# Kernel tuning notes

Measured on AMD Instinct MI355X. Metric: run time of the kernel, lower is better.

The kernel has to match this reference:

```python
import jax, jax.numpy as jnp
import numpy as np

IOU_THR = 0.5
SCORE_THR = 0.05
K = 1000  # fixed NMS candidate budget (padded-ragged replacement for data-dependent shapes)
BBOX_XFORM_CLIP = float(np.log(1000.0 / 16.0))  # torchvision BoxCoder clamp


def setup_inputs() -> dict:
    key = jax.random.key(0)
    k1, k2, k3, k4 = jax.random.split(key, 4)
    B, N, C = 8, 50000, 80
    pred_labels = jax.random.normal(k1, (B, N, C), jnp.float32)
    pred_bboxes = 0.5 * jax.random.normal(k2, (B, N, 4), jnp.float32)
    # anchors: valid xyxy boxes on a ~640px image
    cxy = jax.random.uniform(k3, (B, N, 2), jnp.float32, minval=0.0, maxval=640.0)
    wh = jax.random.uniform(k4, (B, N, 2), jnp.float32, minval=8.0, maxval=128.0)
    anchors = jnp.concatenate([cxy - 0.5 * wh, cxy + 0.5 * wh], axis=-1)
    return {"pred_labels": pred_labels, "pred_bboxes": pred_bboxes, "anchors": anchors}


def _decode_boxes(codes, anchors):
    # torchvision BoxCoder.decode_single with weights (1,1,1,1)
    w = anchors[:, 2] - anchors[:, 0]
    h = anchors[:, 3] - anchors[:, 1]
    cx = anchors[:, 0] + 0.5 * w
    cy = anchors[:, 1] + 0.5 * h
    dx, dy = codes[:, 0], codes[:, 1]
    dw = jnp.minimum(codes[:, 2], BBOX_XFORM_CLIP)
    dh = jnp.minimum(codes[:, 3], BBOX_XFORM_CLIP)
    pcx = dx * w + cx
    pcy = dy * h + cy
    pw = jnp.exp(dw) * w
    ph = jnp.exp(dh) * h
    return jnp.stack([pcx - 0.5 * pw, pcy - 0.5 * ph, pcx + 0.5 * pw, pcy + 0.5 * ph], axis=-1)


def _pairwise_iou(b):
    # b: [K,4] xyxy
    area = (b[:, 2] - b[:, 0]) * (b[:, 3] - b[:, 1])
    lt = jnp.maximum(b[:, None, :2], b[None, :, :2])
    rb = jnp.minimum(b[:, None, 2:], b[None, :, 2:])
    wh = jnp.clip(rb - lt, 0.0)
    inter = wh[..., 0] * wh[..., 1]
    return inter / (area[:, None] + area[None, :] - inter + 1e-9)


def _nms_keep(boxes):
    # boxes already sorted by descending score; greedy suppression
    iou = _pairwise_iou(boxes)
    idx = jnp.arange(K)

    def body(i, keep):
        suppress = (iou[i] > IOU_THR) & (idx > i) & keep[i]
        return keep & ~suppress

    return jax.lax.fori_loop(0, K, body, jnp.ones((K,), bool))


def _decode_image(labels, codes, anchors):
    # labels [N,C], codes [N,4], anchors [N,4]
    probs = jax.nn.sigmoid(labels)
    dt_score = jnp.max(probs, axis=1)
    dt_class = jnp.argmax(probs, axis=1)
    fg = (dt_class != 0) & (dt_score > SCORE_THR)
    masked = jnp.where(fg, dt_score, -1.0)  # background sorts last
    top_s, top_i = jax.lax.top_k(masked, K)
    cls = dt_class[top_i]
    boxes = _decode_boxes(codes[top_i], anchors[top_i])
    keep = _nms_keep(boxes) & (top_s > 0.0)
    out_scores = jnp.where(keep, top_s, 0.0)
    out_boxes = jnp.where(keep[:, None], boxes, 0.0)
    out_cls = jnp.where(keep, cls, -1)
    return out_cls, out_scores, out_boxes, keep


def reference(pred_labels, pred_bboxes, anchors):
    # Padded-ragged analog of the nested_tensor result:
    # category_ids [B,K] int, scores [B,K], bboxes [B,K,4], keep [B,K] validity mask
    return jax.vmap(_decode_image)(pred_labels, pred_bboxes, anchors)
```

## Files before the change

kernel.cpp:

```cpp
#include <hip/hip_runtime.h>
#include <cstdint>
#include <cstddef>

typedef unsigned int u32;
typedef unsigned long long u64;

#define BB   8
#define NN   50000
#define CC   80
#define KTOP 1000
#define CAP  4096
#define NHB  129
#define CLIPV 4.135166556742356f

#define OFF_KEYS 0UL
#define OFF_CLS  1600000UL
#define OFF_HIST 3200000UL
#define OFF_CNT  3204128UL
#define OFF_CAND 3204640UL
#define OFF_TKEY 3466784UL
#define OFF_TIDX 3498784UL
#define OFF_BOX  3530784UL
#define OFF_AREA 3658784UL
#define OFF_MAT  3690784UL

__global__ __launch_bounds__(256) void k_scores_u(const float4* __restrict__ labels4,
                                                  u32* __restrict__ keys,
                                                  int* __restrict__ cls,
                                                  u32* __restrict__ ghist) {
    __shared__ float4 tile[64 * 21];
    __shared__ float  pbest[3][64];
    __shared__ int    pcls[3][64];
    __shared__ u32    lhist[NHB];
    int t = threadIdx.x;
    int img = blockIdx.x / 196;
    int blk = blockIdx.x - img * 196;
    size_t img_base = (size_t)img * NN * 20;
    for (int i = t; i < NHB; i += 256) lhist[i] = 0;
    int a = t & 63;
    int q = t >> 6;
#pragma unroll
    for (int tl = 0; tl < 4; ++tl) {
        int na0 = blk * 256 + tl * 64;
        int nv = NN - na0; if (nv > 64) nv = 64; if (nv < 0) nv = 0;
        int lim = nv * 20;
#pragma unroll
        for (int i = 0; i < 5; ++i) {
            int s = i * 256 + t;
            if (s < lim) {
                float4 v = labels4[img_base + (size_t)na0 * 20 + s];
                tile[s + s / 20] = v;
            }
        }
        __syncthreads();
        float best = -1.0e30f; int bc = 0;
        if (a < nv) {
#pragma unroll
            for (int j = 0; j < 5; ++j) {
                float4 v = tile[a * 21 + q * 5 + j];
                int c = q * 20 + j * 4;
                if (v.x > best) { best = v.x; bc = c; }
                if (v.y > best) { best = v.y; bc = c + 1; }
                if (v.z > best) { best = v.z; bc = c + 2; }
                if (v.w > best) { best = v.w; bc = c + 3; }
            }
            if (q > 0) { pbest[q - 1][a] = best; pcls[q - 1][a] = bc; }
        }
        __syncthreads();
        if (q == 0 && a < nv) {
#pragma unroll
            for (int r = 0; r < 3; ++r) {
                float pb = pbest[r][a];
                if (pb > best) { best = pb; bc = pcls[r][a]; }
            }
            int g = img * NN + na0 + a;
            float score = 1.0f / (1.0f + expf(-best));
            bool fg = (bc != 0) && (score > 0.05f);
            u32 key = fg ? __float_as_uint(score) : 0u;
            keys[g] = key;
            cls[g] = bc;
            u32 kb = key >> 16;
            u32 idx = (kb >= 0x3F00u) ? (kb - 0x3F00u) : 128u;
            atomicAdd(&lhist[idx], 1u);
        }
        __syncthreads();
    }
    for (int i = t; i < NHB; i += 256) {
        u32 c = lhist[i];
        if (c) atomicAdd(&ghist[img * NHB + i], c);
    }
}

__global__ __launch_bounds__(256) void k_gather(const u32* __restrict__ keys,
                                                const u32* __restrict__ ghist,
                                                u32* __restrict__ cnt,
                                                u64* __restrict__ cand) {
    __shared__ u32 wsum[4];
    __shared__ u32 bbase;
    __shared__ u32 sT16;
    __shared__ u32 wtot;
    int t = threadIdx.x;
    int img = blockIdx.x / 196;
    int blk = blockIdx.x - img * 196;

    u32 v = 0;
    if (t < 128) v = ghist[img * NHB + (127 - t)];
    u32 incl = v;
#pragma unroll
    for (int d = 1; d < 64; d <<= 1) {
        u32 up = __shfl_up(incl, (unsigned)d);
        if ((t & 63) >= d) incl += up;
    }
    if (t == 63) wtot = incl;
    __syncthreads();
    if (t >= 64 && t < 128) incl += wtot;
    if (t < 128) {
        u32 excl = incl - v;
        if (excl < KTOP && incl >= KTOP) sT16 = 0x3F00u + 127u - (u32)t;
    }
    if (t == 127 && incl < KTOP) sT16 = 0x3F00u;
    __syncthreads();
    u32 T16 = sT16;

    int n = blk * 256 + t;
    u32 key = 0; bool pass = false;
    if (n < NN) {
        key = keys[img * NN + n];
        pass = (key >> 16) >= T16;
    }
    u64 mask = __ballot(pass);
    int lane = t & 63, wid = t >> 6;
    u32 prefix = (u32)__popcll(mask & ((1ull << lane) - 1ull));
    if (lane == 0) wsum[wid] = (u32)__popcll(mask);
    __syncthreads();
    if (t == 0) {
        u32 s0 = wsum[0], s1 = wsum[1], s2 = wsum[2], s3 = wsum[3];
        u32 tot = s0 + s1 + s2 + s3;
        bbase = tot ? atomicAdd(&cnt[img * 16], tot) : 0u;
        wsum[0] = 0; wsum[1] = s0; wsum[2] = s0 + s1; wsum[3] = s0 + s1 + s2;
    }
    __syncthreads();
    if (pass) {
        u32 pos = bbase + wsum[wid] + prefix;
        if (pos < CAP)
            cand[(size_t)img * CAP + pos] = ((u64)key << 32) | (u32)(~(u32)n);
    }
}

__global__ __launch_bounds__(256) void k_sortA(u64* __restrict__ cand,
                                               const u32* __restrict__ cnt) {
    __shared__ u64 sm[1024];
    int b = blockIdx.x >> 2;
    int c = blockIdx.x & 3;
    int tid = threadIdx.x;
    int m = (int)min(cnt[b * 16], (u32)CAP);
    int base = c * 1024;
    u64* cp = cand + (size_t)b * CAP;
    for (int i = tid; i < 1024; i += 256) {
        int g = base + i;
        sm[i] = (g < m) ? cp[g] : 0ull;
    }
    __syncthreads();
    for (int k = 2; k <= 1024; k <<= 1)
        for (int j = k >> 1; j > 0; j >>= 1) {
            for (int i = tid; i < 1024; i += 256) {
                int ixj = i ^ j;
                if (ixj > i) {
                    bool desc = (((base + i) & k) == 0);
                    u64 x = sm[i], y = sm[ixj];
                    if (desc ? (x < y) : (x > y)) { sm[i] = y; sm[ixj] = x; }
                }
            }
            __syncthreads();
        }
    for (int i = tid; i < 1024; i += 256) cp[base + i] = sm[i];
}

__global__ __launch_bounds__(512) void k_sortB(const u64* __restrict__ cand,
                                               const float4* __restrict__ codes,
                                               const float4* __restrict__ anchors,
                                               u32* __restrict__ tkey, u32* __restrict__ tidx,
                                               float4* __restrict__ boxes, float* __restrict__ area) {
    __shared__ u64 sm[CAP];
    int b = blockIdx.x, tid = threadIdx.x;
    const u64* cp = cand + (size_t)b * CAP;
    for (int i = tid; i < CAP; i += 512) sm[i] = cp[i];
    __syncthreads();
    for (int k = 2048; k <= 4096; k <<= 1)
        for (int j = k >> 1; j > 0; j >>= 1) {
            for (int i = tid; i < CAP; i += 512) {
                int ixj = i ^ j;
                if (ixj > i) {
                    bool desc = ((i & k) == 0);
                    u64 x = sm[i], y = sm[ixj];
                    if (desc ? (x < y) : (x > y)) { sm[i] = y; sm[ixj] = x; }
                }
            }
            __syncthreads();
        }
#pragma unroll
    for (int r = 0; r < 2; ++r) {
        int i = r * 512 + tid;
        if (i < KTOP) {
            u64 v = sm[i];
            u32 kb = (u32)(v >> 32);
            u32 n = ~(u32)v;
            if (kb == 0u) n = 0u;
            int g = b * KTOP + i;
            tkey[g] = kb; tidx[g] = n;
            float4 a = anchors[(size_t)b * NN + n];
            float4 cc = codes[(size_t)b * NN + n];
            float w = a.z - a.x, h = a.w - a.y;
            float cx = a.x + 0.5f * w, cy = a.y + 0.5f * h;
            float dw = fminf(cc.z, CLIPV), dh = fminf(cc.w, CLIPV);
            float pcx = cc.x * w + cx, pcy = cc.y * h + cy;
            float pw = expf(dw) * w, ph = expf(dh) * h;
            float x0 = pcx - 0.5f * pw, y0 = pcy - 0.5f * ph;
            float x1 = pcx + 0.5f * pw, y1 = pcy + 0.5f * ph;
            boxes[g] = make_float4(x0, y0, x1, y1);
            area[g] = (x1 - x0) * (y1 - y0);
        }
    }
}

__global__ __launch_bounds__(256) void k_mat(const float4* __restrict__ boxes,
                                             const float* __restrict__ area,
                                             u64* __restrict__ mat) {
    __shared__ float4 sb[256];
    __shared__ float  sa[256];
    int bid = blockIdx.x;
    int wc = bid & 3, rc = (bid >> 2) & 3, b = bid >> 4;
    int t = threadIdx.x;
    int j0 = wc * 256;
    int jn = min(256, KTOP - j0);
    if (t < jn) { sb[t] = boxes[b * KTOP + j0 + t]; sa[t] = area[b * KTOP + j0 + t]; }
    __syncthreads();
    if (t >= 250) return;
    int i = rc * 250 + t;
    float4 bi = boxes[b * KTOP + i];
    float ai = area[b * KTOP + i];
    u64 w[4] = {0ull, 0ull, 0ull, 0ull};
    int estart = i - j0 + 1; if (estart < 0) estart = 0;
    for (int e = estart; e < jn; ++e) {
        float4 bj = sb[e];
        float lx = fmaxf(bi.x, bj.x), ly = fmaxf(bi.y, bj.y);
        float rx = fminf(bi.z, bj.z), ry = fminf(bi.w, bj.w);
        float ww = fmaxf(rx - lx, 0.0f), hh = fmaxf(ry - ly, 0.0f);
        float inter = ww * hh;
        float iou = inter / (ai + sa[e] - inter + 1e-9f);
        if (iou > 0.5f) w[e >> 6] |= (1ull << (e & 63));
    }
    u64* outp = &mat[((size_t)(b * KTOP + i)) * 16 + wc * 4];
    outp[0] = w[0]; outp[1] = w[1]; outp[2] = w[2]; outp[3] = w[3];
}

__global__ __launch_bounds__(64) void k_nmsout(const u64* __restrict__ mat,
                                               const u32* __restrict__ tkey,
                                               const u32* __restrict__ tidx,
                                               const int* __restrict__ cls,
                                               const float4* __restrict__ boxes,
                                               float* __restrict__ out) {
    __shared__ u64 buf[2][1024];
    __shared__ u64 kws[16];
    int b = blockIdx.x, lane = threadIdx.x;
    const u64* mb = mat + (size_t)b * (KTOP * 16);
#pragma unroll
    for (int r = 0; r < 16; ++r) buf[0][r * 64 + lane] = mb[r * 64 + lane];
    __syncthreads();
    u64 kw = 0;
    if (lane < 15) kw = ~0ull;
    else if (lane == 15) kw = (1ull << 40) - 1;
    for (int p = 0; p < 16; ++p) {
        int cur = p & 1;
        u64 stg[16];
        if (p < 15) {
#pragma unroll
            for (int r = 0; r < 16; ++r) {
                int idx = (p + 1) * 1024 + r * 64 + lane;
                stg[r] = (idx < KTOP * 16) ? mb[idx] : 0ull;
            }
        }
        u64 applied = 0;
        if (lane == p) {
            for (int c = 0; c < 8; ++c) {
                u64 col[8];
#pragma unroll
                for (int qq = 0; qq < 8; ++qq) col[qq] = buf[cur][(c * 8 + qq) * 16 + p];
#pragma unroll
                for (int qq = 0; qq < 8; ++qq) {
                    int e = c * 8 + qq;
                    if ((kw >> e) & 1ull) { kw &= ~col[qq]; applied |= (1ull << e); }
                }
            }
        }
        applied = __shfl(applied, p);
        if (lane > p && lane < 16) {
            for (int c = 0; c < 8; ++c) {
                u64 col[8];
#pragma unroll
                for (int qq = 0; qq < 8; ++qq) col[qq] = buf[cur][(c * 8 + qq) * 16 + lane];
#pragma unroll
                for (int qq = 0; qq < 8; ++qq)
                    if ((applied >> (c * 8 + qq)) & 1ull) kw &= ~col[qq];
            }
        }
        __syncthreads();
        if (p < 15) {
#pragma unroll
            for (int r = 0; r < 16; ++r) buf[cur ^ 1][r * 64 + lane] = stg[r];
            __syncthreads();
        }
    }
    if (lane < 16) kws[lane] = kw;
    __syncthreads();
    const int BK = BB * KTOP;
#pragma unroll
    for (int r = 0; r < 16; ++r) {
        int k = r * 64 + lane;
        if (k < KTOP) {
            int g = b * KTOP + k;
            bool kp = (kws[k >> 6] >> (k & 63)) & 1ull;
            float sc = __uint_as_float(tkey[g]);
            kp = kp && (sc > 0.0f);
            int cl = cls[(size_t)b * NN + tidx[g]];
            float4 bx = boxes[g];
            out[g] = kp ? (float)cl : -1.0f;
            out[BK + g] = kp ? sc : 0.0f;
            float* ob = out + 2 * BK + (size_t)g * 4;
            ob[0] = kp ? bx.x : 0.0f;
            ob[1] = kp ? bx.y : 0.0f;
            ob[2] = kp ? bx.z : 0.0f;
            ob[3] = kp ? bx.w : 0.0f;
            out[6 * BK + g] = kp ? 1.0f : 0.0f;
        }
    }
}

extern "C" void kernel_launch(void* const* d_in, const int* in_sizes, int n_in,
                              void* d_out, int out_size, void* d_ws, size_t ws_size,
                              hipStream_t stream) {
    const float* labels  = (const float*)d_in[0];
    const float* codes   = (const float*)d_in[1];
    const float* anchors = (const float*)d_in[2];
    char* ws = (char*)d_ws;
    u32* keys  = (u32*)(ws + OFF_KEYS);
    int* cls   = (int*)(ws + OFF_CLS);
    u32* hist  = (u32*)(ws + OFF_HIST);
    u32* cnt   = (u32*)(ws + OFF_CNT);
    u64* cand  = (u64*)(ws + OFF_CAND);
    u32* tkey  = (u32*)(ws + OFF_TKEY);
    u32* tidx  = (u32*)(ws + OFF_TIDX);
    float4* bx = (float4*)(ws + OFF_BOX);
    float* ar  = (float*)(ws + OFF_AREA);
    u64* mat   = (u64*)(ws + OFF_MAT);

    hipMemsetAsync(ws + OFF_HIST, 0, OFF_CAND - OFF_HIST, stream);

    k_scores_u<<<BB * 196, 256, 0, stream>>>((const float4*)labels, keys, cls, hist);
    k_gather<<<BB * 196, 256, 0, stream>>>(keys, hist, cnt, cand);
    k_sortA<<<BB * 4, 256, 0, stream>>>(cand, cnt);
    k_sortB<<<BB, 512, 0, stream>>>(cand, (const float4*)codes, (const float4*)anchors,
                                    tkey, tidx, bx, ar);
    k_mat<<<BB * 16, 256, 0, stream>>>(bx, ar, mat);
    k_nmsout<<<BB, 64, 0, stream>>>(mat, tkey, tidx, cls, bx, (float*)d_out);
}
```

Measured before the change: 388.7 us.

## Rewrite greedy NMS scan with wave shuffles and split output into separate kernel

The NMS kernel stops staging the suppression matrix through double-buffered shared memory with single-lane serial scans. Each lane now holds one row in registers, resolves the diagonal 64-bit block with a shuffle-driven greedy loop, and OR-reduces the kept rows' later words across the wave with xor shuffles. Output writing moves into a separate, fully parallel kernel that reads keep words from a new workspace area. The cost is an extra launch plus a serial 64-iteration shuffle loop and 16-word row loads per lane, which are strided in global memory.

```diff
diff --git a/kernel.cpp b/kernel.cpp
--- a/kernel.cpp
+++ b/kernel.cpp
@@ -23,6 +23,7 @@
 #define OFF_BOX  3530784UL
 #define OFF_AREA 3658784UL
 #define OFF_MAT  3690784UL
+#define OFF_KEEP 4714784UL
 
 __global__ __launch_bounds__(256) void k_scores_u(const float4* __restrict__ labels4,
                                                   u32* __restrict__ keys,
@@ -254,86 +255,73 @@
     outp[0] = w[0]; outp[1] = w[1]; outp[2] = w[2]; outp[3] = w[3];
 }
 
-__global__ __launch_bounds__(64) void k_nmsout(const u64* __restrict__ mat,
-                                               const u32* __restrict__ tkey,
-                                               const u32* __restrict__ tidx,
-                                               const int* __restrict__ cls,
-                                               const float4* __restrict__ boxes,
-                                               float* __restrict__ out) {
-    __shared__ u64 buf[2][1024];
-    __shared__ u64 kws[16];
+__global__ __launch_bounds__(64) void k_nms2(const u64* __restrict__ mat,
+                                             u64* __restrict__ keepw) {
     int b = blockIdx.x, lane = threadIdx.x;
     const u64* mb = mat + (size_t)b * (KTOP * 16);
-#pragma unroll
-    for (int r = 0; r < 16; ++r) buf[0][r * 64 + lane] = mb[r * 64 + lane];
-    __syncthreads();
-    u64 kw = 0;
-    if (lane < 15) kw = ~0ull;
-    else if (lane == 15) kw = (1ull << 40) - 1;
+    u64 kw[16];
+#pragma unroll
+    for (int w = 0; w < 15; ++w) kw[w] = ~0ull;
+    kw[15] = (1ull << 40) - 1;
     for (int p = 0; p < 16; ++p) {
-        int cur = p & 1;
-        u64 stg[16];
-        if (p < 15) {
-#pragma unroll
-            for (int r = 0; r < 16; ++r) {
-                int idx = (p + 1) * 1024 + r * 64 + lane;
-                stg[r] = (idx < KTOP * 16) ? mb[idx] : 0ull;
-            }
-        }
+        int row = p * 64 + lane;
+        u64 r[16];
+        if (row < KTOP) {
+            const u64* rp = mb + (size_t)row * 16;
+#pragma unroll
+            for (int w = 0; w < 16; ++w) r[w] = rp[w];
+        } else {
+#pragma unroll
+            for (int w = 0; w < 16; ++w) r[w] = 0ull;
+        }
+        u64 kwp = kw[p];
         u64 applied = 0;
-        if (lane == p) {
-            for (int c = 0; c < 8; ++c) {
-                u64 col[8];
-#pragma unroll
-                for (int qq = 0; qq < 8; ++qq) col[qq] = buf[cur][(c * 8 + qq) * 16 + p];
-#pragma unroll
-                for (int qq = 0; qq < 8; ++qq) {
-                    int e = c * 8 + qq;
-                    if ((kw >> e) & 1ull) { kw &= ~col[qq]; applied |= (1ull << e); }
-                }
-            }
-        }
-        applied = __shfl(applied, p);
-        if (lane > p && lane < 16) {
-            for (int c = 0; c < 8; ++c) {
-                u64 col[8];
-#pragma unroll
-                for (int qq = 0; qq < 8; ++qq) col[qq] = buf[cur][(c * 8 + qq) * 16 + lane];
-#pragma unroll
-                for (int qq = 0; qq < 8; ++qq)
-                    if ((applied >> (c * 8 + qq)) & 1ull) kw &= ~col[qq];
-            }
-        }
-        __syncthreads();
-        if (p < 15) {
-#pragma unroll
-            for (int r = 0; r < 16; ++r) buf[cur ^ 1][r * 64 + lane] = stg[r];
-            __syncthreads();
-        }
-    }
-    if (lane < 16) kws[lane] = kw;
-    __syncthreads();
+        u64 myp = r[p];
+#pragma unroll 1
+        for (int e = 0; e < 64; ++e) {
+            if ((kwp >> e) & 1ull) {
+                u64 s = __shfl(myp, e);
+                kwp &= ~s;
+                applied |= (1ull << e);
+            }
+        }
+        kw[p] = kwp;
+        bool mine = (applied >> lane) & 1ull;
+        for (int w = p + 1; w < 16; ++w) {
+            u64 v = mine ? r[w] : 0ull;
+#pragma unroll
+            for (int d = 32; d > 0; d >>= 1) v |= __shfl_xor(v, d);
+            kw[w] &= ~v;
+        }
+    }
+    if (lane < 16) keepw[b * 16 + lane] = kw[lane];
+}
+
+__global__ __launch_bounds__(256) void k_out(const u64* __restrict__ keepw,
+                                             const u32* __restrict__ tkey,
+                                             const u32* __restrict__ tidx,
+                                             const int* __restrict__ cls,
+                                             const float4* __restrict__ boxes,
+                                             float* __restrict__ out) {
+    int gid = blockIdx.x * 256 + threadIdx.x;
+    if (gid >= BB * KTOP) return;
+    int b = gid / KTOP;
+    int k = gid - b * KTOP;
+    u64 kwv = keepw[b * 16 + (k >> 6)];
+    bool kp = (kwv >> (k & 63)) & 1ull;
+    float sc = __uint_as_float(tkey[gid]);
+    kp = kp && (sc > 0.0f);
+    int cl = cls[(size_t)b * NN + tidx[gid]];
+    float4 bx = boxes[gid];
     const int BK = BB * KTOP;
-#pragma unroll
-    for (int r = 0; r < 16; ++r) {
-        int k = r * 64 + lane;
-        if (k < KTOP) {
-            int g = b * KTOP + k;
-            bool kp = (kws[k >> 6] >> (k & 63)) & 1ull;
-            float sc = __uint_as_float(tkey[g]);
-            kp = kp && (sc > 0.0f);
-            int cl = cls[(size_t)b * NN + tidx[g]];
-            float4 bx = boxes[g];
-            out[g] = kp ? (float)cl : -1.0f;
-            out[BK + g] = kp ? sc : 0.0f;
-            float* ob = out + 2 * BK + (size_t)g * 4;
-            ob[0] = kp ? bx.x : 0.0f;
-            ob[1] = kp ? bx.y : 0.0f;
-            ob[2] = kp ? bx.z : 0.0f;
-            ob[3] = kp ? bx.w : 0.0f;
-            out[6 * BK + g] = kp ? 1.0f : 0.0f;
-        }
-    }
+    out[gid] = kp ? (float)cl : -1.0f;
+    out[BK + gid] = kp ? sc : 0.0f;
+    float* ob = out + 2 * BK + (size_t)gid * 4;
+    ob[0] = kp ? bx.x : 0.0f;
+    ob[1] = kp ? bx.y : 0.0f;
+    ob[2] = kp ? bx.z : 0.0f;
+    ob[3] = kp ? bx.w : 0.0f;
+    out[6 * BK + gid] = kp ? 1.0f : 0.0f;
 }
 
 extern "C" void kernel_launch(void* const* d_in, const int* in_sizes, int n_in,
@@ -353,6 +341,7 @@
     float4* bx = (float4*)(ws + OFF_BOX);
     float* ar  = (float*)(ws + OFF_AREA);
     u64* mat   = (u64*)(ws + OFF_MAT);
+    u64* kpw   = (u64*)(ws + OFF_KEEP);
 
     hipMemsetAsync(ws + OFF_HIST, 0, OFF_CAND - OFF_HIST, stream);
 
@@ -362,5 +351,6 @@
     k_sortB<<<BB, 512, 0, stream>>>(cand, (const float4*)codes, (const float4*)anchors,
                                     tkey, tidx, bx, ar);
     k_mat<<<BB * 16, 256, 0, stream>>>(bx, ar, mat);
-    k_nmsout<<<BB, 64, 0, stream>>>(mat, tkey, tidx, cls, bx, (float*)d_out);
-}
+    k_nms2<<<BB, 64, 0, stream>>>(mat, kpw);
+    k_out<<<(BB * KTOP + 255) / 256, 256, 0, stream>>>(kpw, tkey, tidx, cls, bx, (float*)d_out);
+}
```

Result: slower. 435.2 us (+12.0%).
